# Optimization experiments

Hardware: AMD Instinct MI355X
Metric: run time of the kernel (lower is better)

## Reference

```python
import jax, jax.numpy as jnp
import numpy as np

H = 8          # head_count
C = 512        # emb_dim
DH = C // H    # head_emb_size = 64
FF = 4 * C     # feed_forward hidden = 2048
EPS = 1e-5     # nn.LayerNorm default eps


def setup_inputs() -> dict:
    key = jax.random.key(0)
    ks = jax.random.split(key, 16)
    s = lambda fan_in: 1.0 / np.sqrt(fan_in)
    inp = {
        "x": jax.random.normal(ks[0], (4, 2048, C), dtype=jnp.float32),
        "ln1_g": jnp.ones((C,), jnp.float32),
        "ln1_b": jnp.zeros((C,), jnp.float32),
        # per-head QKV projections, stacked over heads: [H, C, DH]
        "Wq": jax.random.uniform(ks[1], (H, C, DH), jnp.float32, -s(C), s(C)),
        "bq": jax.random.uniform(ks[2], (H, DH), jnp.float32, -s(C), s(C)),
        "Wk": jax.random.uniform(ks[3], (H, C, DH), jnp.float32, -s(C), s(C)),
        "bk": jax.random.uniform(ks[4], (H, DH), jnp.float32, -s(C), s(C)),
        "Wv": jax.random.uniform(ks[5], (H, C, DH), jnp.float32, -s(C), s(C)),
        "bv": jax.random.uniform(ks[6], (H, DH), jnp.float32, -s(C), s(C)),
        "Wp": jax.random.uniform(ks[7], (C, C), jnp.float32, -s(C), s(C)),
        "bp": jax.random.uniform(ks[8], (C,), jnp.float32, -s(C), s(C)),
        "ln2_g": jnp.ones((C,), jnp.float32),
        "ln2_b": jnp.zeros((C,), jnp.float32),
        "W1": jax.random.uniform(ks[9], (C, FF), jnp.float32, -s(C), s(C)),
        "b1": jax.random.uniform(ks[10], (FF,), jnp.float32, -s(C), s(C)),
        "W2": jax.random.uniform(ks[11], (FF, C), jnp.float32, -s(FF), s(FF)),
        "b2": jax.random.uniform(ks[12], (C,), jnp.float32, -s(FF), s(FF)),
    }
    return inp


def _layernorm(x, g, b):
    mu = jnp.mean(x, axis=-1, keepdims=True)
    var = jnp.mean((x - mu) ** 2, axis=-1, keepdims=True)
    return (x - mu) * jax.lax.rsqrt(var + EPS) * g + b


def _block(x, ln1_g, ln1_b, Wq, bq, Wk, bk, Wv, bv, Wp, bp, ln2_g, ln2_b, W1, b1, W2, b2):
    B, T, _ = x.shape
    h = _layernorm(x, ln1_g, ln1_b)
    # per-head projections, vectorized over heads: [B,H,T,DH]
    Q = jnp.einsum("btc,hcd->bhtd", h, Wq) + bq[None, :, None, :]
    K = jnp.einsum("btc,hcd->bhtd", h, Wk) + bk[None, :, None, :]
    V = jnp.einsum("btc,hcd->bhtd", h, Wv) + bv[None, :, None, :]
    wei = jnp.einsum("bhtd,bhsd->bhts", Q, K) / jnp.sqrt(jnp.float32(DH))
    causal = jnp.tril(jnp.ones((T, T), dtype=bool))
    wei = jnp.where(causal, wei, jnp.float32(-1e9))  # masked_fill(-1e9)
    wei = jax.nn.softmax(wei, axis=-1)
    out = jnp.einsum("bhts,bhsd->bhtd", wei, V)      # [B,H,T,DH]
    # concat heads (head order = ModuleList order) -> [B,T,C]
    out = out.transpose(0, 2, 1, 3).reshape(B, T, H * DH)
    attn = out @ Wp + bp
    x = x + attn
    h2 = _layernorm(x, ln2_g, ln2_b)
    ff = jax.nn.relu(h2 @ W1 + b1) @ W2 + b2
    return x + ff


def reference(x, ln1_g, ln1_b, Wq, bq, Wk, bk, Wv, bv, Wp, bp, ln2_g, ln2_b, W1, b1, W2, b2):
    return _block(x, ln1_g, ln1_b, Wq, bq, Wk, bk, Wv, bv, Wp, bp, ln2_g, ln2_b, W1, b1, W2, b2)
```

## Files before the change

### kernel.cpp

```cpp
#include <hip/hip_runtime.h>

typedef unsigned short u16;
typedef unsigned int   u32;
typedef __attribute__((ext_vector_type(4))) int   i32x4;
typedef __attribute__((ext_vector_type(4))) float f32x4;
typedef __attribute__((ext_vector_type(4))) unsigned short u16x4;
typedef __attribute__((ext_vector_type(8))) unsigned short u16x8;

#define DEVI static __device__ __forceinline__

DEVI u16 f2b(float f) {
  u32 u = __builtin_bit_cast(u32, f);
  return (u16)((u + 0x7FFFu + ((u >> 16) & 1u)) >> 16);
}

DEVI float exp2_hw(float x) {
  float r;
  asm("v_exp_f32 %0, %1" : "=v"(r) : "v"(x));
  return r;
}

DEVI void mfma16(f32x4& d, i32x4 a, i32x4 b) {
  asm("v_mfma_f32_16x16x32_bf16 %0, %1, %2, %0" : "+v"(d) : "v"(a), "v"(b));
}

DEVI void gload16(const void* g, void* l) {
  __builtin_amdgcn_global_load_lds(
      (const __attribute__((address_space(1))) void*)g,
      (__attribute__((address_space(3))) void*)l, 16, 0, 0);
}

DEVI int swz(int row, int b) {
  return (row << 7) + (((b >> 4) ^ (row & 7)) << 4) + (b & 15);
}

__global__ __launch_bounds__(256) void trans_tile(
    const float* __restrict__ src, u16* __restrict__ dst, int R, int C)
{
  __shared__ u16 tile[64][72];
  const int rb = blockIdx.x * 64, cb = blockIdx.y * 64;
  const int t = threadIdx.x;
  const int tr = t >> 2, tc = (t & 3) * 16;
  const float* sp = src + (size_t)(rb + tr) * C + cb + tc;
  #pragma unroll
  for (int q = 0; q < 4; q++) {
    float4 v = *(const float4*)(sp + q * 4);
    tile[tr][tc + q*4 + 0] = f2b(v.x);
    tile[tr][tc + q*4 + 1] = f2b(v.y);
    tile[tr][tc + q*4 + 2] = f2b(v.z);
    tile[tr][tc + q*4 + 3] = f2b(v.w);
  }
  __syncthreads();
  const int dc = t >> 2, dr = (t & 3) * 16;
  u16x8 o0, o1;
  #pragma unroll
  for (int j = 0; j < 8; j++) { o0[j] = tile[dr + j][dc]; o1[j] = tile[dr + 8 + j][dc]; }
  u16* dp = dst + (size_t)(cb + dc) * R + rb + dr;
  *(u16x8*)(dp) = o0;
  *(u16x8*)(dp + 8) = o1;
}

__global__ __launch_bounds__(256) void pack_qkv_tile(
    const float* __restrict__ Wq, const float* __restrict__ Wk,
    const float* __restrict__ Wv, u16* __restrict__ dst)
{
  __shared__ u16 tile[64][72];
  const int bid = blockIdx.x;
  const int cb = (bid & 7) * 64, h = (bid >> 3) & 7, widx = bid >> 6;
  const float* W = (widx == 0) ? Wq : (widx == 1) ? Wk : Wv;
  const float* src = W + (size_t)h * 512 * 64;
  const int t = threadIdx.x;
  const int tr = t >> 2, tc = (t & 3) * 16;
  const float* sp = src + (size_t)(cb + tr) * 64 + tc;
  #pragma unroll
  for (int q = 0; q < 4; q++) {
    float4 v = *(const float4*)(sp + q * 4);
    tile[tr][tc + q*4 + 0] = f2b(v.x);
    tile[tr][tc + q*4 + 1] = f2b(v.y);
    tile[tr][tc + q*4 + 2] = f2b(v.z);
    tile[tr][tc + q*4 + 3] = f2b(v.w);
  }
  __syncthreads();
  const int dc = t >> 2, dr = (t & 3) * 16;
  u16x8 o0, o1;
  #pragma unroll
  for (int j = 0; j < 8; j++) { o0[j] = tile[dr + j][dc]; o1[j] = tile[dr + 8 + j][dc]; }
  u16* dp = dst + (size_t)(widx * 512 + h * 64 + dc) * 512 + cb + dr;
  *(u16x8*)(dp) = o0;
  *(u16x8*)(dp + 8) = o1;
}

__global__ __launch_bounds__(256) void ln_kernel(
    const float* __restrict__ x, const float* __restrict__ gamma,
    const float* __restrict__ beta, u16* __restrict__ out)
{
  const int lane = threadIdx.x & 63;
  const int row = blockIdx.x * 4 + (threadIdx.x >> 6);
  const float4* xr = (const float4*)(x + (size_t)row * 512) + lane * 2;
  float4 a0 = xr[0], a1 = xr[1];
  float s  = a0.x + a0.y + a0.z + a0.w + a1.x + a1.y + a1.z + a1.w;
  float sq = a0.x*a0.x + a0.y*a0.y + a0.z*a0.z + a0.w*a0.w
           + a1.x*a1.x + a1.y*a1.y + a1.z*a1.z + a1.w*a1.w;
  #pragma unroll
  for (int o = 32; o > 0; o >>= 1) { s += __shfl_xor(s, o); sq += __shfl_xor(sq, o); }
  const float mu = s * (1.0f / 512.0f);
  const float rstd = rsqrtf(sq * (1.0f / 512.0f) - mu * mu + 1e-5f);
  const float4* g4 = (const float4*)gamma + lane * 2;
  const float4* b4 = (const float4*)beta  + lane * 2;
  float4 g0 = g4[0], g1 = g4[1], b0 = b4[0], b1 = b4[1];
  float xv[8] = {a0.x,a0.y,a0.z,a0.w,a1.x,a1.y,a1.z,a1.w};
  float gv[8] = {g0.x,g0.y,g0.z,g0.w,g1.x,g1.y,g1.z,g1.w};
  float bv[8] = {b0.x,b0.y,b0.z,b0.w,b1.x,b1.y,b1.z,b1.w};
  u16x8 ov;
  #pragma unroll
  for (int j = 0; j < 8; j++) ov[j] = f2b((xv[j] - mu) * rstd * gv[j] + bv[j]);
  *(u16x8*)(out + (size_t)row * 512 + lane * 8) = ov;
}

template<int KD, int NT, int EPI>
__global__ __launch_bounds__(256) void gemm_bt(
    const u16* __restrict__ A, const u16* __restrict__ Bt,
    const float* __restrict__ bias0, const float* __restrict__ bias1,
    const float* __restrict__ bias2, const float* __restrict__ resid,
    void* __restrict__ out0, void* __restrict__ out1, void* __restrict__ out2)
{
  __shared__ __align__(16) u16 sA[3][128 * 32];
  __shared__ __align__(16) u16 sB[3][128 * 32];
  constexpr int NSTEP = KD / 32;
  const int tid = threadIdx.x, lane = tid & 63, w = tid >> 6;
  const int m0 = (blockIdx.x & 63) * 128, n0 = (blockIdx.x >> 6) * 128;
  const int wr = w >> 1, wc = w & 1, r = lane & 15, gq = lane >> 4;

  f32x4 acc[4][4] = {};

  const int o0 = w * 2048 + lane * 16;
  const int row0 = o0 >> 6, kb0 = o0 & 63;
  const int o1 = o0 + 1024;
  const int row1 = o1 >> 6, kb1 = o1 & 63;
  const char* Ab = (const char*)A;
  const char* Bb = (const char*)Bt;

#define STAGE(step, buf) do {                                                \
    const int kbyte_ = (step) * 64;                                          \
    char* sAd_ = (char*)sA + (buf) * 8192 + w * 2048;                        \
    char* sBd_ = (char*)sB + (buf) * 8192 + w * 2048;                        \
    gload16(Ab + (size_t)(m0 + row0) * (KD * 2) + kbyte_ + kb0, sAd_);       \
    gload16(Ab + (size_t)(m0 + row1) * (KD * 2) + kbyte_ + kb1, sAd_ + 1024);\
    gload16(Bb + (size_t)(n0 + row0) * (KD * 2) + kbyte_ + kb0, sBd_);       \
    gload16(Bb + (size_t)(n0 + row1) * (KD * 2) + kbyte_ + kb1, sBd_ + 1024);\
  } while (0)

  STAGE(0, 0);
  STAGE(1, 1);

  for (int t = 0; t < NSTEP; t++) {
    __builtin_amdgcn_sched_barrier(0);
    __builtin_amdgcn_s_barrier();
    if (t + 2 < NSTEP) {
      STAGE(t + 2, (t + 2) % 3);
      asm volatile("s_waitcnt vmcnt(8)" ::: "memory");
    } else if (t + 1 < NSTEP) {
      asm volatile("s_waitcnt vmcnt(4)" ::: "memory");
    } else {
      asm volatile("s_waitcnt vmcnt(0)" ::: "memory");
    }
    __builtin_amdgcn_sched_barrier(0);
    __builtin_amdgcn_s_barrier();
    const u16* sAc = sA[t % 3];
    const u16* sBc = sB[t % 3];
    i32x4 af[4], bfr[4];
    #pragma unroll
    for (int i = 0; i < 4; i++)
      af[i] = *(const i32x4*)(sAc + (wr * 64 + i * 16 + r) * 32 + gq * 8);
    #pragma unroll
    for (int j = 0; j < 4; j++)
      bfr[j] = *(const i32x4*)(sBc + (wc * 64 + j * 16 + r) * 32 + gq * 8);
    __builtin_amdgcn_s_setprio(1);
    #pragma unroll
    for (int i = 0; i < 4; i++)
      #pragma unroll
      for (int j = 0; j < 4; j++)
        mfma16(acc[i][j], af[i], bfr[j]);
    __builtin_amdgcn_s_setprio(0);
  }
#undef STAGE

  #pragma unroll
  for (int i = 0; i < 4; i++) {
    #pragma unroll
    for (int j = 0; j < 4; j++) {
      const int mb = m0 + wr * 64 + i * 16 + gq * 4;
      const int nc = n0 + wc * 64 + j * 16 + r;
      #pragma unroll
      for (int e = 0; e < 4; e++) {
        const int m = mb + e;
        float v = acc[i][j][e];
        if (EPI == 0) {
          float bias; u16* dst;
          if (nc < 512)       { bias = bias0[nc];        dst = (u16*)out0; }
          else if (nc < 1024) { bias = bias1[nc - 512];  dst = (u16*)out1; }
          else                { bias = bias2[nc - 1024]; dst = (u16*)out2; }
          v += bias;
          const int nn = nc & 511, h = nn >> 6, d = nn & 63;
          const int bb = m >> 11, tt = m & 2047;
          dst[(size_t)((bb * 8 + h) * 2048 + tt) * 64 + d] = f2b(v);
        } else if (EPI == 1) {
          v += bias0[nc] + resid[(size_t)m * 512 + nc];
          ((float*)out0)[(size_t)m * 512 + nc] = v;
        } else {
          v += bias0[nc];
          v = fmaxf(v, 0.0f);
          ((u16*)out0)[(size_t)m * 2048 + nc] = f2b(v);
        }
      }
    }
  }
}

__global__ __launch_bounds__(256) void attn_kernel(
    const u16* __restrict__ Q, const u16* __restrict__ K,
    const u16* __restrict__ V, u16* __restrict__ O)
{
  __shared__ __align__(16) char lds[40960];
  const int tid = threadIdx.x, lane = tid & 63, w = tid >> 6;
  const int bh = blockIdx.x & 31, i = blockIdx.x >> 5;
  const int s = i & 7, g = i >> 3;
  const int qt = (g == 0) ? s : (g == 1) ? (15 - s) : (g == 2) ? (16 + s) : (31 - s);
  const int r = lane & 15, gq = lane >> 4;
  const u16* Qb = Q + (size_t)bh * (2048 * 64);
  const u16* Kb = K + (size_t)bh * (2048 * 64);
  const u16* Vb = V + (size_t)bh * (2048 * 64);
  const int bb = bh >> 3, hh = bh & 7;
  char* Pb = lds + 32768 + w * 2048;

  const int sv = (tid & 15) * 4;
  const int dv = (tid >> 4) * 4;
  u16x4 vr[4];
  const float SC2 = 0.125f * 1.44269504f;

#define STAGEK(s0g, buf) do {                                              \
    _Pragma("unroll")                                                      \
    for (int i_ = 0; i_ < 2; i_++) {                                       \
      int o_ = w * 2048 + i_ * 1024 + lane * 16;                           \
      int so_ = o_ ^ (((o_ >> 7) & 7) << 4);                               \
      gload16((const char*)(Kb + (size_t)(s0g) * 64) + so_,                \
              lds + (buf) * 8192 + w * 2048 + i_ * 1024);                  \
    } } while (0)

#define LOADV(s0g) do {                                                    \
    _Pragma("unroll")                                                      \
    for (int j_ = 0; j_ < 4; j_++)                                         \
      vr[j_] = *(const u16x4*)(Vb + (size_t)((s0g) + sv + j_) * 64 + dv);  \
    } while (0)

#define WRITEV(buf) do {                                                   \
    _Pragma("unroll")                                                      \
    for (int dd_ = 0; dd_ < 4; dd_++) {                                    \
      u16x4 val_ = {vr[0][dd_], vr[1][dd_], vr[2][dd_], vr[3][dd_]};       \
      *(u16x4*)(lds + 16384 + (buf) * 8192 + swz(dv + dd_, sv * 2)) = val_;\
    } } while (0)

  const int q0 = qt << 6;
  const int qg = q0 + w * 16 + r;

  i32x4 qf[2];
  qf[0] = *(const i32x4*)(Qb + (size_t)(q0 + w * 16 + r) * 64 + gq * 8);
  qf[1] = *(const i32x4*)(Qb + (size_t)(q0 + w * 16 + r) * 64 + 32 + gq * 8);

  STAGEK(0, 0);
  LOADV(0);
  WRITEV(0);
  __syncthreads();

  f32x4 accO[4] = {};
  float m_run = -1e30f, l_run = 0.0f;

  for (int t = 0; t <= qt; t++) {
    const int cb = t & 1, nb = cb ^ 1;
    const bool diag = (t == qt);
    const int s0 = t << 6;
    if (!diag) {
      STAGEK(s0 + 64, nb);
      LOADV(s0 + 64);
    }

    f32x4 st[4] = {};
    const int sbmax = diag ? (w + 1) : 4;
    #pragma unroll
    for (int kd = 0; kd < 2; kd++)
      #pragma unroll
      for (int sb = 0; sb < 4; sb++)
        if (sb < sbmax) {
          i32x4 kf = *(const i32x4*)(lds + cb * 8192 + swz(sb * 16 + r, kd * 64 + gq * 16));
          mfma16(st[sb], kf, qf[kd]);
        }

    float tmax = -1e30f;
    if (diag) {
      #pragma unroll
      for (int sb = 0; sb < 4; sb++)
        #pragma unroll
        for (int e = 0; e < 4; e++) {
          int sg = s0 + sb * 16 + gq * 4 + e;
          float v = st[sb][e] * SC2;
          v = (sg <= qg) ? v : -1e30f;
          st[sb][e] = v;
          tmax = fmaxf(tmax, v);
        }
    } else {
      #pragma unroll
      for (int sb = 0; sb < 4; sb++)
        #pragma unroll
        for (int e = 0; e < 4; e++) {
          float v = st[sb][e] * SC2;
          st[sb][e] = v;
          tmax = fmaxf(tmax, v);
        }
    }
    tmax = fmaxf(tmax, __shfl_xor(tmax, 16));
    tmax = fmaxf(tmax, __shfl_xor(tmax, 32));

    if (!__all(tmax <= m_run)) {
      const float mnew = fmaxf(m_run, tmax);
      const float alpha = exp2_hw(m_run - mnew);
      l_run *= alpha;
      float ae[4];
      #pragma unroll
      for (int e = 0; e < 4; e++) ae[e] = __shfl(alpha, gq * 4 + e);
      #pragma unroll
      for (int db = 0; db < 4; db++)
        #pragma unroll
        for (int e = 0; e < 4; e++) accO[db][e] *= ae[e];
      m_run = mnew;
    }
    float rsum = 0.0f;
    #pragma unroll
    for (int sb = 0; sb < 4; sb++)
      #pragma unroll
      for (int e = 0; e < 4; e++) {
        float pv = exp2_hw(st[sb][e] - m_run);
        st[sb][e] = pv;
        rsum += pv;
      }
    rsum += __shfl_xor(rsum, 16);
    rsum += __shfl_xor(rsum, 32);
    l_run += rsum;

    #pragma unroll
    for (int sb = 0; sb < 4; sb++) {
      u32 lo, hi;
      asm("v_cvt_pk_bf16_f32 %0, %1, %2" : "=v"(lo) : "v"(st[sb][0]), "v"(st[sb][1]));
      asm("v_cvt_pk_bf16_f32 %0, %1, %2" : "=v"(hi) : "v"(st[sb][2]), "v"(st[sb][3]));
      uint2 pk; pk.x = lo; pk.y = hi;
      *(uint2*)(Pb + swz(r, sb * 32 + gq * 8)) = pk;
    }

    const int kmax = diag ? ((w >> 1) + 1) : 2;
    #pragma unroll
    for (int ks = 0; ks < 2; ks++)
      if (ks < kmax) {
        i32x4 pf = *(const i32x4*)(Pb + swz(r, ks * 64 + gq * 16));
        #pragma unroll
        for (int db = 0; db < 4; db++) {
          i32x4 vf = *(const i32x4*)(lds + 16384 + cb * 8192 + swz(db * 16 + r, ks * 64 + gq * 16));
          mfma16(accO[db], pf, vf);
        }
      }

    if (!diag) WRITEV(nb);
    __syncthreads();
  }

  float le[4];
  #pragma unroll
  for (int e = 0; e < 4; e++) le[e] = 1.0f / __shfl(l_run, gq * 4 + e);
  #pragma unroll
  for (int db = 0; db < 4; db++)
    #pragma unroll
    for (int e = 0; e < 4; e++) {
      int qrow = q0 + w * 16 + gq * 4 + e;
      int d = db * 16 + r;
      O[(size_t)(bb * 2048 + qrow) * 512 + hh * 64 + d] = f2b(accO[db][e] * le[e]);
    }
#undef STAGEK
#undef LOADV
#undef WRITEV
}

extern "C" void kernel_launch(void* const* d_in, const int* in_sizes, int n_in,
                              void* d_out, int out_size, void* d_ws, size_t ws_size,
                              hipStream_t stream)
{
  const float* x    = (const float*)d_in[0];
  const float* ln1g = (const float*)d_in[1];
  const float* ln1b = (const float*)d_in[2];
  const float* Wq   = (const float*)d_in[3];
  const float* bq   = (const float*)d_in[4];
  const float* Wk   = (const float*)d_in[5];
  const float* bk   = (const float*)d_in[6];
  const float* Wv   = (const float*)d_in[7];
  const float* bv   = (const float*)d_in[8];
  const float* Wp   = (const float*)d_in[9];
  const float* bp   = (const float*)d_in[10];
  const float* ln2g = (const float*)d_in[11];
  const float* ln2b = (const float*)d_in[12];
  const float* W1   = (const float*)d_in[13];
  const float* b1   = (const float*)d_in[14];
  const float* W2   = (const float*)d_in[15];
  const float* b2   = (const float*)d_in[16];

  char* ws = (char*)d_ws;
  const size_t MB = 1ull << 20;
  float* x1  = (float*)(ws);
  u16* hbuf  = (u16*)(ws + 16 * MB);
  u16* Qb    = (u16*)(ws + 24 * MB);
  u16* Kb    = (u16*)(ws + 32 * MB);
  u16* Vb    = (u16*)(ws + 40 * MB);
  u16* attn  = (u16*)(ws + 48 * MB);
  u16* fbuf  = (u16*)(ws + 24 * MB);
  u16* Wqkv  = (u16*)(ws + 56 * MB);
  u16* Wpt   = (u16*)(ws + 58 * MB);
  u16* W1t   = (u16*)(ws + 59 * MB);
  u16* W2t   = (u16*)(ws + 61 * MB);
  float* outf = (float*)d_out;

  pack_qkv_tile<<<192, 256, 0, stream>>>(Wq, Wk, Wv, Wqkv);
  trans_tile<<<dim3(8, 8),  256, 0, stream>>>(Wp, Wpt, 512, 512);
  trans_tile<<<dim3(8, 32), 256, 0, stream>>>(W1, W1t, 512, 2048);
  trans_tile<<<dim3(32, 8), 256, 0, stream>>>(W2, W2t, 2048, 512);
  ln_kernel<<<2048, 256, 0, stream>>>(x, ln1g, ln1b, hbuf);
  gemm_bt<512, 12, 0><<<768, 256, 0, stream>>>(hbuf, Wqkv, bq, bk, bv,
                                               nullptr, Qb, Kb, Vb);
  attn_kernel<<<1024, 256, 0, stream>>>(Qb, Kb, Vb, attn);
  gemm_bt<512, 4, 1><<<256, 256, 0, stream>>>(attn, Wpt, bp, nullptr, nullptr,
                                              x, x1, nullptr, nullptr);
  ln_kernel<<<2048, 256, 0, stream>>>(x1, ln2g, ln2b, hbuf);
  gemm_bt<512, 16, 2><<<1024, 256, 0, stream>>>(hbuf, W1t, b1, nullptr, nullptr,
                                                nullptr, fbuf, nullptr, nullptr);
  gemm_bt<2048, 4, 1><<<256, 256, 0, stream>>>(fbuf, W2t, b2, nullptr, nullptr,
                                               x1, outf, nullptr, nullptr);
}
```

Measured before the change: 178.4 us.

## Keep attention P in registers via transposed PV MFMA; drop GEMM setprio

```diff
diff --git a/kernel.cpp b/kernel.cpp
--- a/kernel.cpp
+++ b/kernel.cpp
@@ -175,13 +175,11 @@
     #pragma unroll
     for (int j = 0; j < 4; j++)
       bfr[j] = *(const i32x4*)(sBc + (wc * 64 + j * 16 + r) * 32 + gq * 8);
-    __builtin_amdgcn_s_setprio(1);
     #pragma unroll
     for (int i = 0; i < 4; i++)
       #pragma unroll
       for (int j = 0; j < 4; j++)
         mfma16(acc[i][j], af[i], bfr[j]);
-    __builtin_amdgcn_s_setprio(0);
   }
 #undef STAGE
 
@@ -221,7 +219,7 @@
     const u16* __restrict__ Q, const u16* __restrict__ K,
     const u16* __restrict__ V, u16* __restrict__ O)
 {
-  __shared__ __align__(16) char lds[40960];
+  __shared__ __align__(16) char lds[32768];
   const int tid = threadIdx.x, lane = tid & 63, w = tid >> 6;
   const int bh = blockIdx.x & 31, i = blockIdx.x >> 5;
   const int s = i & 7, g = i >> 3;
@@ -231,7 +229,6 @@
   const u16* Kb = K + (size_t)bh * (2048 * 64);
   const u16* Vb = V + (size_t)bh * (2048 * 64);
   const int bb = bh >> 3, hh = bh & 7;
-  char* Pb = lds + 32768 + w * 2048;
 
   const int sv = (tid & 15) * 4;
   const int dv = (tid >> 4) * 4;
@@ -324,13 +321,10 @@
       const float mnew = fmaxf(m_run, tmax);
       const float alpha = exp2_hw(m_run - mnew);
       l_run *= alpha;
-      float ae[4];
-      #pragma unroll
-      for (int e = 0; e < 4; e++) ae[e] = __shfl(alpha, gq * 4 + e);
       #pragma unroll
       for (int db = 0; db < 4; db++)
         #pragma unroll
-        for (int e = 0; e < 4; e++) accO[db][e] *= ae[e];
+        for (int e = 0; e < 4; e++) accO[db][e] *= alpha;
       m_run = mnew;
     }
     float rsum = 0.0f;
@@ -346,24 +340,22 @@
     rsum += __shfl_xor(rsum, 32);
     l_run += rsum;
 
-    #pragma unroll
-    for (int sb = 0; sb < 4; sb++) {
-      u32 lo, hi;
-      asm("v_cvt_pk_bf16_f32 %0, %1, %2" : "=v"(lo) : "v"(st[sb][0]), "v"(st[sb][1]));
-      asm("v_cvt_pk_bf16_f32 %0, %1, %2" : "=v"(hi) : "v"(st[sb][2]), "v"(st[sb][3]));
-      uint2 pk; pk.x = lo; pk.y = hi;
-      *(uint2*)(Pb + swz(r, sb * 32 + gq * 8)) = pk;
-    }
-
     const int kmax = diag ? ((w >> 1) + 1) : 2;
     #pragma unroll
     for (int ks = 0; ks < 2; ks++)
       if (ks < kmax) {
-        i32x4 pf = *(const i32x4*)(Pb + swz(r, ks * 64 + gq * 16));
+        u32 w0, w1, w2, w3;
+        asm("v_cvt_pk_bf16_f32 %0, %1, %2" : "=v"(w0) : "v"(st[2*ks][0]),   "v"(st[2*ks][1]));
+        asm("v_cvt_pk_bf16_f32 %0, %1, %2" : "=v"(w1) : "v"(st[2*ks][2]),   "v"(st[2*ks][3]));
+        asm("v_cvt_pk_bf16_f32 %0, %1, %2" : "=v"(w2) : "v"(st[2*ks+1][0]), "v"(st[2*ks+1][1]));
+        asm("v_cvt_pk_bf16_f32 %0, %1, %2" : "=v"(w3) : "v"(st[2*ks+1][2]), "v"(st[2*ks+1][3]));
+        i32x4 pf = {(int)w0, (int)w1, (int)w2, (int)w3};
         #pragma unroll
         for (int db = 0; db < 4; db++) {
-          i32x4 vf = *(const i32x4*)(lds + 16384 + cb * 8192 + swz(db * 16 + r, ks * 64 + gq * 16));
-          mfma16(accO[db], pf, vf);
+          uint2 a0 = *(const uint2*)(lds + 16384 + cb * 8192 + swz(db * 16 + r, ks * 64 + gq * 8));
+          uint2 a1 = *(const uint2*)(lds + 16384 + cb * 8192 + swz(db * 16 + r, ks * 64 + gq * 8 + 32));
+          i32x4 vfr = {(int)a0.x, (int)a0.y, (int)a1.x, (int)a1.y};
+          mfma16(accO[db], vfr, pf);
         }
       }
 
@@ -371,17 +363,15 @@
     __syncthreads();
   }
 
-  float le[4];
-  #pragma unroll
-  for (int e = 0; e < 4; e++) le[e] = 1.0f / __shfl(l_run, gq * 4 + e);
-  #pragma unroll
-  for (int db = 0; db < 4; db++)
-    #pragma unroll
-    for (int e = 0; e < 4; e++) {
-      int qrow = q0 + w * 16 + gq * 4 + e;
-      int d = db * 16 + r;
-      O[(size_t)(bb * 2048 + qrow) * 512 + hh * 64 + d] = f2b(accO[db][e] * le[e]);
-    }
+  const float li = 1.0f / l_run;
+  const int qrow = q0 + w * 16 + r;
+  #pragma unroll
+  for (int db = 0; db < 4; db++) {
+    u16x4 ov;
+    #pragma unroll
+    for (int e = 0; e < 4; e++) ov[e] = f2b(accO[db][e] * li);
+    *(u16x4*)(O + (size_t)(bb * 2048 + qrow) * 512 + hh * 64 + db * 16 + gq * 4) = ov;
+  }
 #undef STAGEK
 #undef LOADV
 #undef WRITEV
```

New measurement: 176.2 us. No clear change (-1.2%).
